# Kernel tuning notes

Hardware: AMD Instinct MI355X
Metric: run time of the kernel (lower is better)

The kernel has to match this reference:

```python
import jax, jax.numpy as jnp
import numpy as np

# Dimensions: B point clouds of S points each, C channels, H heads of dim D
B, S, C, H, D = 8, 2048, 128, 4, 32
EPS = 1e-5  # GroupNorm eps (torch default)


def setup_inputs() -> dict:
    key = jax.random.key(0)
    ks = jax.random.split(key, 3)
    x = jax.random.normal(ks[0], (B, S, C), dtype=jnp.float32)
    # GroupNorm(num_groups=1) affine params (per-channel)
    gamma = jnp.ones((C,), dtype=jnp.float32)
    beta = jnp.zeros((C,), dtype=jnp.float32)
    # to_qkv: 1x1 Minkowski conv == linear, no bias; output = 3*H*D channels
    w_qkv = jax.random.normal(ks[1], (3 * H * D, C), dtype=jnp.float32) * 0.02
    # to_out: 1x1 conv with bias, H*D -> C
    w_out = jax.random.normal(ks[2], (C, H * D), dtype=jnp.float32) * 0.02
    b_out = jnp.zeros((C,), dtype=jnp.float32)
    return {"x": x, "gamma": gamma, "beta": beta, "w_qkv": w_qkv,
            "w_out": w_out, "b_out": b_out}


def reference(x, gamma, beta, w_qkv, w_out, b_out):
    scale = D ** -0.5
    # GroupNorm(num_groups=1) applied per cloud over ALL channels and points
    mu = jnp.mean(x, axis=(1, 2), keepdims=True)
    var = jnp.var(x, axis=(1, 2), keepdims=True)
    nx = (x - mu) * jax.lax.rsqrt(var + EPS) * gamma + beta  # [B,S,C]
    # Pointwise qkv projection (no bias)
    qkv = jnp.einsum('bsc,fc->bsf', nx, w_qkv)  # [B,S,3*H*D]
    q, k, v = jnp.split(qkv, 3, axis=-1)
    q = q.reshape(B, S, H, D) * scale
    k = k.reshape(B, S, H, D)
    v = v.reshape(B, S, H, D)
    # Per-cloud multi-head self-attention (block-diagonal over clouds)
    attn = jax.nn.softmax(jnp.einsum('bihd,bjhd->bhij', q, k), axis=-1)  # [B,H,S,S]
    o = jnp.einsum('bhij,bjhd->bihd', attn, v).reshape(B, S, H * D)
    # Output projection (with bias) + residual
    return jnp.einsum('bsf,cf->bsc', o, w_out) + b_out + x
```

## Files before the change

kernel.cpp:

```cpp
#include <hip/hip_runtime.h>
#include <hip/hip_bf16.h>

#define B_ 8
#define S_ 2048
#define C_ 128
#define H_ 4
#define D_ 32
#define SC_ (S_*C_)
#define HD_ (H_*D_)

typedef short bf16x8 __attribute__((ext_vector_type(8)));
typedef float f32x4 __attribute__((ext_vector_type(4)));
union FragU { uint4 u; bf16x8 h; };

__device__ __forceinline__ unsigned short f2bf(float f) {
  __hip_bfloat16 h = __float2bfloat16(f);
  return *reinterpret_cast<unsigned short*>(&h);
}
__device__ __forceinline__ unsigned int pk2t(float a, float b) {
  union { float f; unsigned int u; } ua, ub;
  ua.f = a; ub.f = b;
  return __builtin_amdgcn_perm(ub.u, ua.u, 0x07060302u);
}
__device__ __forceinline__ unsigned int pk2r(float a, float b) {
  return (unsigned int)f2bf(a) | ((unsigned int)f2bf(b) << 16);
}
#define EXP2(x) __builtin_amdgcn_exp2f(x)

__global__ __launch_bounds__(256) void k_stats1(const float* __restrict__ x,
                                                const float* __restrict__ wqkv,
                                                const float* __restrict__ wout,
                                                float* __restrict__ part,
                                                unsigned short* __restrict__ wq_bf,
                                                unsigned short* __restrict__ wo_bf) {
  __shared__ float ssum[256], ssq[256];
  int b = blockIdx.x >> 5, sl = blockIdx.x & 31;
  int tid = threadIdx.x;
  int gid = blockIdx.x * 256 + tid;
  if (gid < 16384) {
    int e = gid * 4;
    const float4 u = (e < 49152) ? *(const float4*)(wqkv + e) : *(const float4*)(wout + e - 49152);
    unsigned short tv[4] = {f2bf(u.x), f2bf(u.y), f2bf(u.z), f2bf(u.w)};
    unsigned short* dst = (e < 49152) ? (wq_bf + e) : (wo_bf + e - 49152);
    *(uint2*)dst = *(uint2*)tv;
  }
  const float4* xp = (const float4*)(x + (size_t)b * SC_);
  float sum = 0.f, sq = 0.f;
  for (int i = sl * 2048 + tid; i < (sl + 1) * 2048; i += 256) {
    float4 u = xp[i];
    sum += u.x + u.y + u.z + u.w;
    sq  += u.x*u.x + u.y*u.y + u.z*u.z + u.w*u.w;
  }
  ssum[tid] = sum; ssq[tid] = sq;
  __syncthreads();
  for (int s = 128; s > 0; s >>= 1) {
    if (tid < s) { ssum[tid] += ssum[tid + s]; ssq[tid] += ssq[tid + s]; }
    __syncthreads();
  }
  if (tid == 0) { part[blockIdx.x * 2] = ssum[0]; part[blockIdx.x * 2 + 1] = ssq[0]; }
}

__global__ __launch_bounds__(512) void k_qkv(const float* __restrict__ x,
                                             const float* __restrict__ gamma,
                                             const float* __restrict__ beta,
                                             const unsigned short* __restrict__ wq_bf,
                                             const float* __restrict__ part,
                                             unsigned short* __restrict__ q_ws,
                                             unsigned short* __restrict__ k_ws,
                                             unsigned short* __restrict__ v_ws) {
  __shared__ __align__(16) unsigned short Nls[32][136];
  __shared__ float gs[128], bs[128];
  __shared__ float st2[2];
  const int tid = threadIdx.x;
  const int w = tid >> 6, l = tid & 63, g = l >> 4, i = l & 15;
  const int gr0 = blockIdx.x * 32;
  const int b = gr0 >> 11;
  if (tid < 128) { gs[tid] = gamma[tid]; bs[tid] = beta[tid]; }
  if (tid < 32) {
    float s1 = part[(b * 32 + tid) * 2];
    float s2 = part[(b * 32 + tid) * 2 + 1];
    #pragma unroll
    for (int m = 16; m >= 1; m >>= 1) { s1 += __shfl_xor(s1, m); s2 += __shfl_xor(s2, m); }
    if (tid == 0) {
      float mu = s1 / (float)SC_;
      float var = s2 / (float)SC_ - mu * mu;
      st2[0] = mu; st2[1] = rsqrtf(var + 1e-5f);
    }
  }
  __syncthreads();
  const float mu = st2[0], rstd = st2[1];
  {
    const float4* xp = (const float4*)(x + (size_t)gr0 * C_);
    #pragma unroll
    for (int t = 0; t < 2; ++t) {
      int e = tid + t * 512;
      float4 u = xp[e];
      int r = e >> 5, c0 = (e & 31) * 4;
      float4 gv = *(const float4*)&gs[c0];
      float4 bv = *(const float4*)&bs[c0];
      unsigned short tv[4] = {
        f2bf((u.x - mu) * rstd * gv.x + bv.x),
        f2bf((u.y - mu) * rstd * gv.y + bv.y),
        f2bf((u.z - mu) * rstd * gv.z + bv.z),
        f2bf((u.w - mu) * rstd * gv.w + bv.w)};
      *(uint2*)&Nls[r][c0] = *(uint2*)tv;
    }
  }
  __syncthreads();
  f32x4 acc[2][3];
  #pragma unroll
  for (int rt = 0; rt < 2; ++rt)
    #pragma unroll
    for (int n = 0; n < 3; ++n) acc[rt][n] = (f32x4){0.f,0.f,0.f,0.f};

  #pragma unroll
  for (int kk = 0; kk < 4; ++kk) {
    FragU bfr[3];
    #pragma unroll
    for (int n = 0; n < 3; ++n)
      bfr[n].u = *(const uint4*)(wq_bf + (size_t)((w * 3 + n) * 16 + i) * 128 + kk * 32 + 8 * g);
    FragU af[2];
    #pragma unroll
    for (int rt = 0; rt < 2; ++rt) af[rt].u = *(const uint4*)&Nls[rt * 16 + i][kk * 32 + 8 * g];
    #pragma unroll
    for (int n = 0; n < 3; ++n)
      #pragma unroll
      for (int rt = 0; rt < 2; ++rt)
        acc[rt][n] = __builtin_amdgcn_mfma_f32_16x16x32_bf16(af[rt].h, bfr[n].h, acc[rt][n], 0, 0, 0);
  }
  __syncthreads();
  unsigned short (*Vbuf)[32] = (unsigned short(*)[32])&Nls[0][0];

  const float SCQ = 0.17677669529663687f * 1.4426950408889634f;
  const int base64 = ((blockIdx.x & 63) >> 1) * 64;
  const int odd32 = (blockIdx.x & 1) * 32;
  #pragma unroll
  for (int n = 0; n < 3; ++n) {
    int f = (w * 3 + n) * 16 + i;
    int which = f >> 7, fi = f & 127, h = fi >> 5, dd = fi & 31;
    #pragma unroll
    for (int rt = 0; rt < 2; ++rt) {
      if (which == 2) {
        *(unsigned int*)&Vbuf[fi][8 * g + 4 * rt]     = pk2r(acc[rt][n][0], acc[rt][n][1]);
        *(unsigned int*)&Vbuf[fi][8 * g + 4 * rt + 2] = pk2r(acc[rt][n][2], acc[rt][n][3]);
      } else {
        #pragma unroll
        for (int r = 0; r < 4; ++r) {
          int s = (gr0 + rt * 16 + 4 * g + r) & (S_ - 1);
          if (which == 0) {
            q_ws[(((size_t)b * H_ + h) * S_ + s) * D_ + dd] = f2bf(acc[rt][n][r] * SCQ);
          } else {
            k_ws[(((size_t)b * H_ + h) * S_ + s) * D_ + dd] = f2bf(acc[rt][n][r]);
          }
        }
      }
    }
  }
  __syncthreads();
  {
    int fi = tid >> 2, ch = tid & 3;
    int h = fi >> 5, dd = fi & 31;
    uint4 vv = *(const uint4*)&Vbuf[fi][ch * 8];
    *(uint4*)(v_ws + (((size_t)b * H_ + h) * D_ + dd) * S_ + base64 + odd32 + ch * 8) = vv;
  }
}

__global__ __launch_bounds__(512) void k_attn(const unsigned short* __restrict__ qg,
                                              const unsigned short* __restrict__ kg,
                                              const unsigned short* __restrict__ vg,
                                              unsigned short* __restrict__ og) {
  __shared__ __align__(16) unsigned short Kls[2][128][40];
  __shared__ __align__(16) unsigned short Vt[2][32][136];
  const int tid = threadIdx.x;
  const int w = tid >> 6, l = tid & 63;
  const int g = l >> 4, i = l & 15;
  const int qb = blockIdx.x, h = blockIdx.y, b = blockIdx.z;
  const size_t base = ((size_t)b * H_ + h) * (size_t)(S_ * D_);

  FragU qf;
  qf.u = *(const uint4*)(qg + base + (size_t)(qb * 128 + w * 16 + i) * D_ + 8 * g);
  FragU onef;
  onef.u = (uint4){0x3F803F80u, 0x3F803F80u, 0x3F803F80u, 0x3F803F80u};

  const int kr = tid >> 2, kc = tid & 3;
  const int vr = tid >> 4, vc = tid & 15;
  const uint4* kp = (const uint4*)(kg + base);
  const unsigned short* vt = vg + base;

  f32x4 oac[2] = {{0.f,0.f,0.f,0.f},{0.f,0.f,0.f,0.f}};
  f32x4 sac = {0.f,0.f,0.f,0.f};

  *(uint4*)&Kls[0][kr][kc * 8] = kp[kr * 4 + kc];
  *(uint4*)&Vt[0][vr][vc * 8]  = *(const uint4*)(vt + (size_t)vr * S_ + vc * 8);

  for (int kt = 0; kt < 16; ++kt) {
    const int cur = kt & 1;
    __syncthreads();
    uint4 nk, nv;
    const bool pf = kt < 15;
    if (pf) {
      nk = kp[((kt + 1) * 128 + kr) * 4 + kc];
      nv = *(const uint4*)(vt + (size_t)vr * S_ + (kt + 1) * 128 + vc * 8);
    }
    #pragma unroll
    for (int sub = 0; sub < 2; ++sub) {
      f32x4 sf[4];
      __builtin_amdgcn_s_setprio(1);
      #pragma unroll
      for (int n = 0; n < 4; ++n) {
        FragU kf; kf.u = *(const uint4*)&Kls[cur][sub * 64 + n * 16 + i][8 * g];
        f32x4 z = {0.f, 0.f, 0.f, 0.f};
        sf[n] = __builtin_amdgcn_mfma_f32_16x16x32_bf16(kf.h, qf.h, z, 0, 0, 0);
      }
      __builtin_amdgcn_s_setprio(0);
      FragU pa0, pa1;
      pa0.u = (uint4){pk2t(EXP2(sf[0][0]), EXP2(sf[0][1])),
                      pk2t(EXP2(sf[0][2]), EXP2(sf[0][3])),
                      pk2t(EXP2(sf[1][0]), EXP2(sf[1][1])),
                      pk2t(EXP2(sf[1][2]), EXP2(sf[1][3]))};
      pa1.u = (uint4){pk2t(EXP2(sf[2][0]), EXP2(sf[2][1])),
                      pk2t(EXP2(sf[2][2]), EXP2(sf[2][3])),
                      pk2t(EXP2(sf[3][0]), EXP2(sf[3][1])),
                      pk2t(EXP2(sf[3][2]), EXP2(sf[3][3]))};
      __builtin_amdgcn_s_setprio(1);
      sac = __builtin_amdgcn_mfma_f32_16x16x32_bf16(pa0.h, onef.h, sac, 0, 0, 0);
      #pragma unroll
      for (int n = 0; n < 2; ++n) {
        FragU vf; vf.u = *(const uint4*)&Vt[cur][n * 16 + i][sub * 64 + 8 * g];
        oac[n] = __builtin_amdgcn_mfma_f32_16x16x32_bf16(pa0.h, vf.h, oac[n], 0, 0, 0);
      }
      sac = __builtin_amdgcn_mfma_f32_16x16x32_bf16(pa1.h, onef.h, sac, 0, 0, 0);
      #pragma unroll
      for (int n = 0; n < 2; ++n) {
        FragU vf; vf.u = *(const uint4*)&Vt[cur][n * 16 + i][sub * 64 + 32 + 8 * g];
        oac[n] = __builtin_amdgcn_mfma_f32_16x16x32_bf16(pa1.h, vf.h, oac[n], 0, 0, 0);
      }
      __builtin_amdgcn_s_setprio(0);
    }
    if (pf) {
      *(uint4*)&Kls[cur ^ 1][kr][kc * 8] = nk;
      *(uint4*)&Vt[cur ^ 1][vr][vc * 8]  = nv;
    }
  }
  #pragma unroll
  for (int n = 0; n < 2; ++n) {
    #pragma unroll
    for (int r = 0; r < 4; ++r) {
      size_t row = (size_t)qb * 128 + w * 16 + 4 * g + r;
      og[((size_t)b * S_ + row) * HD_ + h * D_ + n * 16 + i] = f2bf(oac[n][r] / sac[r]);
    }
  }
}

__global__ __launch_bounds__(512) void k_out(const unsigned short* __restrict__ o,
                                             const unsigned short* __restrict__ wo_bf,
                                             const float* __restrict__ bo,
                                             const float* __restrict__ x,
                                             float* __restrict__ out) {
  const int tid = threadIdx.x;
  const int w = tid >> 6, l = tid & 63, g = l >> 4, i = l & 15;
  const int gr0 = blockIdx.x * 32;
  const int c = w * 16 + i;
  f32x4 acc[2] = {{0,0,0,0},{0,0,0,0}};
  #pragma unroll
  for (int kk = 0; kk < 4; ++kk) {
    FragU bfr;
    bfr.u = *(const uint4*)(wo_bf + (size_t)c * HD_ + kk * 32 + 8 * g);
    #pragma unroll
    for (int rt = 0; rt < 2; ++rt) {
      FragU af;
      af.u = *(const uint4*)(o + (size_t)(gr0 + rt * 16 + i) * HD_ + kk * 32 + 8 * g);
      acc[rt] = __builtin_amdgcn_mfma_f32_16x16x32_bf16(af.h, bfr.h, acc[rt], 0, 0, 0);
    }
  }
  float bias = bo[c];
  #pragma unroll
  for (int rt = 0; rt < 2; ++rt) {
    #pragma unroll
    for (int r = 0; r < 4; ++r) {
      size_t idx = (size_t)(gr0 + rt * 16 + 4 * g + r) * C_ + c;
      out[idx] = acc[rt][r] + bias + x[idx];
    }
  }
}

extern "C" void kernel_launch(void* const* d_in, const int* in_sizes, int n_in,
                              void* d_out, int out_size, void* d_ws, size_t ws_size,
                              hipStream_t stream) {
  const float* x     = (const float*)d_in[0];
  const float* gamma = (const float*)d_in[1];
  const float* beta  = (const float*)d_in[2];
  const float* wqkv  = (const float*)d_in[3];
  const float* wout  = (const float*)d_in[4];
  const float* bout  = (const float*)d_in[5];
  float* out = (float*)d_out;

  float* part  = (float*)((char*)d_ws + 64);
  unsigned short* wq_bf = (unsigned short*)((char*)d_ws + 4096);
  unsigned short* wo_bf = wq_bf + 49152;
  unsigned short* q_ws = (unsigned short*)((char*)d_ws + 4096 + 98304 + 32768);
  const size_t per = (size_t)B_ * H_ * S_ * D_;
  unsigned short* k_ws = q_ws + per;
  unsigned short* v_ws = k_ws + per;
  unsigned short* o_ws = v_ws + per;

  hipLaunchKernelGGL(k_stats1, dim3(256), dim3(256), 0, stream, x, wqkv, wout, part, wq_bf, wo_bf);
  hipLaunchKernelGGL(k_qkv, dim3(512), dim3(512), 0, stream,
                     x, gamma, beta, wq_bf, part, q_ws, k_ws, v_ws);
  hipLaunchKernelGGL(k_attn, dim3(S_ / 128, H_, B_), dim3(512), 0, stream,
                     q_ws, k_ws, v_ws, o_ws);
  hipLaunchKernelGGL(k_out, dim3(512), dim3(512), 0, stream,
                     o_ws, wo_bf, bout, x, out);
}
```

Before: 53.40 us.

## Fuse GroupNorm stats into QKV kernel using cooperative grid sync

Merges the separate statistics kernel into the QKV projection kernel, which is now launched cooperatively. Each block reduces its own 32-row tile, writes partial sums, waits on a grid-wide barrier, then reduces the 64 partials for its cloud. The x tile stays in registers, so x is read once instead of twice and one kernel launch is removed. In exchange it adds a grid sync, and all 512 blocks must be resident at once.

```diff
diff --git a/kernel.cpp b/kernel.cpp
--- a/kernel.cpp
+++ b/kernel.cpp
@@ -1,5 +1,8 @@
 #include <hip/hip_runtime.h>
 #include <hip/hip_bf16.h>
+#include <hip/hip_cooperative_groups.h>
+
+namespace cg = cooperative_groups;
 
 #define B_ 8
 #define S_ 2048
@@ -27,16 +30,28 @@
 }
 #define EXP2(x) __builtin_amdgcn_exp2f(x)
 
-__global__ __launch_bounds__(256) void k_stats1(const float* __restrict__ x,
-                                                const float* __restrict__ wqkv,
-                                                const float* __restrict__ wout,
-                                                float* __restrict__ part,
-                                                unsigned short* __restrict__ wq_bf,
-                                                unsigned short* __restrict__ wo_bf) {
-  __shared__ float ssum[256], ssq[256];
-  int b = blockIdx.x >> 5, sl = blockIdx.x & 31;
-  int tid = threadIdx.x;
-  int gid = blockIdx.x * 256 + tid;
+__global__ __launch_bounds__(512) void k_qkv(const float* __restrict__ x,
+                                             const float* __restrict__ gamma,
+                                             const float* __restrict__ beta,
+                                             const float* __restrict__ wqkv,
+                                             const float* __restrict__ wout,
+                                             float* __restrict__ part,
+                                             unsigned short* __restrict__ wq_bf,
+                                             unsigned short* __restrict__ wo_bf,
+                                             unsigned short* __restrict__ q_ws,
+                                             unsigned short* __restrict__ k_ws,
+                                             unsigned short* __restrict__ v_ws) {
+  __shared__ __align__(16) unsigned short Nls[32][136];
+  __shared__ float gs[128], bs[128];
+  __shared__ float st2[2];
+  __shared__ float red[16];
+  const int tid = threadIdx.x;
+  const int w = tid >> 6, l = tid & 63, g = l >> 4, i = l & 15;
+  const int bid = blockIdx.x;
+  const int gr0 = bid * 32;
+  const int b = gr0 >> 11;
+
+  int gid = bid * 512 + tid;
   if (gid < 16384) {
     int e = gid * 4;
     const float4 u = (e < 49152) ? *(const float4*)(wqkv + e) : *(const float4*)(wout + e - 49152);
@@ -44,43 +59,39 @@
     unsigned short* dst = (e < 49152) ? (wq_bf + e) : (wo_bf + e - 49152);
     *(uint2*)dst = *(uint2*)tv;
   }
-  const float4* xp = (const float4*)(x + (size_t)b * SC_);
+  if (tid < 128) { gs[tid] = gamma[tid]; bs[tid] = beta[tid]; }
+
+  float4 xr[2];
   float sum = 0.f, sq = 0.f;
-  for (int i = sl * 2048 + tid; i < (sl + 1) * 2048; i += 256) {
-    float4 u = xp[i];
-    sum += u.x + u.y + u.z + u.w;
-    sq  += u.x*u.x + u.y*u.y + u.z*u.z + u.w*u.w;
-  }
-  ssum[tid] = sum; ssq[tid] = sq;
-  __syncthreads();
-  for (int s = 128; s > 0; s >>= 1) {
-    if (tid < s) { ssum[tid] += ssum[tid + s]; ssq[tid] += ssq[tid + s]; }
-    __syncthreads();
-  }
-  if (tid == 0) { part[blockIdx.x * 2] = ssum[0]; part[blockIdx.x * 2 + 1] = ssq[0]; }
-}
-
-__global__ __launch_bounds__(512) void k_qkv(const float* __restrict__ x,
-                                             const float* __restrict__ gamma,
-                                             const float* __restrict__ beta,
-                                             const unsigned short* __restrict__ wq_bf,
-                                             const float* __restrict__ part,
-                                             unsigned short* __restrict__ q_ws,
-                                             unsigned short* __restrict__ k_ws,
-                                             unsigned short* __restrict__ v_ws) {
-  __shared__ __align__(16) unsigned short Nls[32][136];
-  __shared__ float gs[128], bs[128];
-  __shared__ float st2[2];
-  const int tid = threadIdx.x;
-  const int w = tid >> 6, l = tid & 63, g = l >> 4, i = l & 15;
-  const int gr0 = blockIdx.x * 32;
-  const int b = gr0 >> 11;
-  if (tid < 128) { gs[tid] = gamma[tid]; bs[tid] = beta[tid]; }
-  if (tid < 32) {
-    float s1 = part[(b * 32 + tid) * 2];
-    float s2 = part[(b * 32 + tid) * 2 + 1];
-    #pragma unroll
-    for (int m = 16; m >= 1; m >>= 1) { s1 += __shfl_xor(s1, m); s2 += __shfl_xor(s2, m); }
+  {
+    const float4* xp = (const float4*)(x + (size_t)gr0 * C_);
+    #pragma unroll
+    for (int t = 0; t < 2; ++t) {
+      xr[t] = xp[tid + t * 512];
+      sum += xr[t].x + xr[t].y + xr[t].z + xr[t].w;
+      sq  += xr[t].x*xr[t].x + xr[t].y*xr[t].y + xr[t].z*xr[t].z + xr[t].w*xr[t].w;
+    }
+  }
+  {
+    float s1 = sum, s2 = sq;
+    #pragma unroll
+    for (int m = 32; m >= 1; m >>= 1) { s1 += __shfl_xor(s1, m); s2 += __shfl_xor(s2, m); }
+    if (l == 0) { red[w * 2] = s1; red[w * 2 + 1] = s2; }
+  }
+  __syncthreads();
+  if (tid == 0) {
+    float a = 0.f, c = 0.f;
+    #pragma unroll
+    for (int j = 0; j < 8; ++j) { a += red[j * 2]; c += red[j * 2 + 1]; }
+    part[bid * 2] = a; part[bid * 2 + 1] = c;
+  }
+  cg::this_grid().sync();
+
+  if (tid < 64) {
+    const float2 p = *(const float2*)(part + ((bid >> 6) << 7) + tid * 2);
+    float s1 = p.x, s2 = p.y;
+    #pragma unroll
+    for (int m = 32; m >= 1; m >>= 1) { s1 += __shfl_xor(s1, m); s2 += __shfl_xor(s2, m); }
     if (tid == 0) {
       float mu = s1 / (float)SC_;
       float var = s2 / (float)SC_ - mu * mu;
@@ -89,22 +100,18 @@
   }
   __syncthreads();
   const float mu = st2[0], rstd = st2[1];
-  {
-    const float4* xp = (const float4*)(x + (size_t)gr0 * C_);
-    #pragma unroll
-    for (int t = 0; t < 2; ++t) {
-      int e = tid + t * 512;
-      float4 u = xp[e];
-      int r = e >> 5, c0 = (e & 31) * 4;
-      float4 gv = *(const float4*)&gs[c0];
-      float4 bv = *(const float4*)&bs[c0];
-      unsigned short tv[4] = {
-        f2bf((u.x - mu) * rstd * gv.x + bv.x),
-        f2bf((u.y - mu) * rstd * gv.y + bv.y),
-        f2bf((u.z - mu) * rstd * gv.z + bv.z),
-        f2bf((u.w - mu) * rstd * gv.w + bv.w)};
-      *(uint2*)&Nls[r][c0] = *(uint2*)tv;
-    }
+  #pragma unroll
+  for (int t = 0; t < 2; ++t) {
+    int e = tid + t * 512;
+    int r = e >> 5, c0 = (e & 31) * 4;
+    float4 gv = *(const float4*)&gs[c0];
+    float4 bv = *(const float4*)&bs[c0];
+    unsigned short tv[4] = {
+      f2bf((xr[t].x - mu) * rstd * gv.x + bv.x),
+      f2bf((xr[t].y - mu) * rstd * gv.y + bv.y),
+      f2bf((xr[t].z - mu) * rstd * gv.z + bv.z),
+      f2bf((xr[t].w - mu) * rstd * gv.w + bv.w)};
+    *(uint2*)&Nls[r][c0] = *(uint2*)tv;
   }
   __syncthreads();
   f32x4 acc[2][3];
@@ -132,8 +139,8 @@
   unsigned short (*Vbuf)[32] = (unsigned short(*)[32])&Nls[0][0];
 
   const float SCQ = 0.17677669529663687f * 1.4426950408889634f;
-  const int base64 = ((blockIdx.x & 63) >> 1) * 64;
-  const int odd32 = (blockIdx.x & 1) * 32;
+  const int base64 = ((bid & 63) >> 1) * 64;
+  const int odd32 = (bid & 1) * 32;
   #pragma unroll
   for (int n = 0; n < 3; ++n) {
     int f = (w * 3 + n) * 16 + i;
@@ -295,18 +302,19 @@
   const float* bout  = (const float*)d_in[5];
   float* out = (float*)d_out;
 
-  float* part  = (float*)((char*)d_ws + 64);
-  unsigned short* wq_bf = (unsigned short*)((char*)d_ws + 4096);
+  float* part = (float*)d_ws;
+  unsigned short* wq_bf = (unsigned short*)((char*)d_ws + 8192);
   unsigned short* wo_bf = wq_bf + 49152;
-  unsigned short* q_ws = (unsigned short*)((char*)d_ws + 4096 + 98304 + 32768);
+  unsigned short* q_ws  = (unsigned short*)((char*)d_ws + 147456);
   const size_t per = (size_t)B_ * H_ * S_ * D_;
   unsigned short* k_ws = q_ws + per;
   unsigned short* v_ws = k_ws + per;
   unsigned short* o_ws = v_ws + per;
 
-  hipLaunchKernelGGL(k_stats1, dim3(256), dim3(256), 0, stream, x, wqkv, wout, part, wq_bf, wo_bf);
-  hipLaunchKernelGGL(k_qkv, dim3(512), dim3(512), 0, stream,
-                     x, gamma, beta, wq_bf, part, q_ws, k_ws, v_ws);
+  void* qkv_args[] = {(void*)&x, (void*)&gamma, (void*)&beta, (void*)&wqkv, (void*)&wout,
+                      (void*)&part, (void*)&wq_bf, (void*)&wo_bf,
+                      (void*)&q_ws, (void*)&k_ws, (void*)&v_ws};
+  hipLaunchCooperativeKernel((const void*)k_qkv, dim3(512), dim3(512), qkv_args, 0, stream);
   hipLaunchKernelGGL(k_attn, dim3(S_ / 128, H_, B_), dim3(512), 0, stream,
                      q_ws, k_ws, v_ws, o_ws);
   hipLaunchKernelGGL(k_out, dim3(512), dim3(512), 0, stream,
```

Result: slower. 97.16 us (+82.0%).
